# Kernel tuning notes

Measured on AMD Instinct MI355X. Metric: run time of the kernel, lower is better.

## Reference

```python
import jax, jax.numpy as jnp
import numpy as np

B, S, H = 16, 1024, 1024  # S must equal H for the original bmm to type-check


def setup_inputs() -> dict:
    key = jax.random.key(0)
    k1, k2, k3, k4, k5 = jax.random.split(key, 5)
    ht = jax.random.normal(k1, (B, H), dtype=jnp.float32)
    encoder_out = jax.random.normal(k2, (B, S, H), dtype=jnp.float32)
    # nn.Linear(2H, H): weight [H, 2H], bias [H]
    W_attn = jax.random.normal(k3, (H, 2 * H), dtype=jnp.float32) / np.sqrt(2 * H)
    b_attn = jax.random.normal(k4, (H,), dtype=jnp.float32) * 0.01
    # nn.Linear(H, 1, bias=False): weight [1, H]  (computed in forward but its output is discarded)
    W_v = jax.random.normal(k5, (1, H), dtype=jnp.float32) / np.sqrt(H)
    return {"ht": ht, "encoder_out": encoder_out, "W_attn": W_attn, "b_attn": b_attn, "W_v": W_v}


def reference(ht, encoder_out, W_attn, b_attn, W_v):
    b, s, h = encoder_out.shape
    # ht.repeat(S,1,1).transpose(0,1) -> [B,S,H]
    ht_rep = jnp.broadcast_to(ht[:, None, :], (b, s, h))
    energy = jnp.concatenate([ht_rep, encoder_out], axis=2)          # [B,S,2H]
    energy = jnp.tanh(jnp.einsum('bsk,hk->bsh', energy, W_attn) + b_attn)  # [B,S,H]
    # v projection is computed in the original forward but not returned (dead output)
    _attention = jnp.einsum('bsh,oh->bso', energy, W_v)[..., 0]      # [B,S], unused
    # NOTE: softmax over dim=1 (the seq axis) of the full 3D energy, as in the original
    attention_weights = jax.nn.softmax(energy, axis=1)               # [B,S,H]
    # bmm([B,S,H],[B,S,H]) with S==H: contract weights' H axis vs encoder_out's S axis
    context = jnp.einsum('bsk,bkh->bsh', attention_weights, encoder_out)  # [B,S,H]
    return (context, attention_weights)
```

## Files before the change

kernel.cpp:

```cpp
#include <hip/hip_runtime.h>
#include <math.h>

#define Bn 16
#define Sn 1024
#define Hn 1024
static const size_t SH = (size_t)Sn * Hn;
static const size_t BSH = (size_t)Bn * Sn * Hn;

typedef __attribute__((ext_vector_type(8))) short short8;
typedef __attribute__((ext_vector_type(4))) float f32x4;

#define GLD16(gp, lp) __builtin_amdgcn_global_load_lds( \
    (const __attribute__((address_space(1))) void*)(gp), \
    (__attribute__((address_space(3))) void*)(lp), 16, 0, 0)

__device__ __forceinline__ short bfr(float f) {
  union { float f; unsigned u; } v; v.f = f;
  unsigned r = (v.u + 0x7FFFu + ((v.u >> 16) & 1u)) >> 16;
  return (short)r;
}
__device__ __forceinline__ float b2f(unsigned short u) {
  union { unsigned u; float f; } v; v.u = (unsigned)u << 16; return v.f;
}
__device__ __forceinline__ short8 cvt8(float4 x, float4 y) {
  short8 r;
  r[0] = bfr(x.x); r[1] = bfr(x.y); r[2] = bfr(x.z); r[3] = bfr(x.w);
  r[4] = bfr(y.x); r[5] = bfr(y.y); r[6] = bfr(y.z); r[7] = bfr(y.w);
  return r;
}

__device__ __forceinline__ int swz8(int row, int g) {
  return (g & ~7) | ((g & 7) ^ (row & 7));
}

__global__ __launch_bounds__(256) void fused_cvt_kernel(const float* __restrict__ enc,
                                                        short* __restrict__ enc_bf,
                                                        short* __restrict__ encT) {
  __shared__ float tile[64][65];
  const int b = blockIdx.z;
  const int s0 = blockIdx.y * 64, h0 = blockIdx.x * 64;
  const int t = threadIdx.x;
  const int tr = t >> 4, tc = t & 15;
  const float* src = enc + (size_t)b * SH;
#pragma unroll
  for (int i = 0; i < 4; ++i) {
    const int s = i * 16 + tr;
    const float4 v = *(const float4*)(src + (size_t)(s0 + s) * 1024 + h0 + tc * 4);
    tile[s][tc * 4 + 0] = v.x; tile[s][tc * 4 + 1] = v.y;
    tile[s][tc * 4 + 2] = v.z; tile[s][tc * 4 + 3] = v.w;
  }
  __syncthreads();
  {
    const int rloc = t >> 2;
    const int rg = b * 1024 + s0 + rloc;
#pragma unroll
    for (int jj = 0; jj < 2; ++jj) {
      const int jloc = (t & 3) * 2 + jj;
      const int slot = jloc ^ (rg & 7);
      const float4 x = *(const float4*)&tile[rloc][jloc * 8];
      const float4 y = *(const float4*)&tile[rloc][jloc * 8 + 4];
      *(short8*)(enc_bf + (size_t)rg * 1024 + h0 + slot * 8) = cvt8(x, y);
    }
  }
  {
    const int hr = t >> 2, cs = t & 3;
    const int h = h0 + hr;
#pragma unroll
    for (int blk = 0; blk < 2; ++blk) {
      const int sg = blk * 4 + cs;
      const int gl = (s0 >> 3) + sg;
      const int gst = swz8(h, gl);
      short8 pk;
#pragma unroll
      for (int j = 0; j < 8; ++j) pk[j] = bfr(tile[sg * 8 + j][hr]);
      *(short8*)(encT + (size_t)b * SH + (size_t)h * 1024 + gst * 8) = pk;
    }
  }
}

__global__ __launch_bounds__(256) void cvt_enc_kernel(const float* __restrict__ enc,
                                                      short* __restrict__ enc_bf) {
  const int g = blockIdx.x * 256 + threadIdx.x;
  const int row = g >> 7;
  const int cs = g & 127;
  const float4 x = *(const float4*)(enc + (size_t)row * 1024 + cs * 8);
  const float4 y = *(const float4*)(enc + (size_t)row * 1024 + cs * 8 + 4);
  *(short8*)(enc_bf + (size_t)row * 1024 + swz8(row, cs) * 8) = cvt8(x, y);
}

__global__ __launch_bounds__(256) void cvt_w2_kernel(const float* __restrict__ W_attn,
                                                     short* __restrict__ W2_bf) {
  const int g = blockIdx.x * 256 + threadIdx.x;
  const int h = g >> 7;
  const int cs = g & 127;
  const float4 x = *(const float4*)(W_attn + (size_t)h * 2048 + 1024 + cs * 8);
  const float4 y = *(const float4*)(W_attn + (size_t)h * 2048 + 1024 + cs * 8 + 4);
  *(short8*)(W2_bf + (size_t)h * 1024 + swz8(h, cs) * 8) = cvt8(x, y);
}

__global__ __launch_bounds__(256) void c1_kernel(const float* __restrict__ ht,
                                                 const float* __restrict__ W_attn,
                                                 const float* __restrict__ b_attn,
                                                 float* __restrict__ c1) {
  __shared__ float hts[16384];
  const int t = threadIdx.x;
#pragma unroll
  for (int i = 0; i < 16; ++i)
    *(float4*)&hts[i * 1024 + t * 4] = *(const float4*)&ht[i * 1024 + t * 4];
  __syncthreads();
  const int h = blockIdx.x * 4 + (t >> 6);
  const int lane = t & 63;
  const float* w = W_attn + (size_t)h * 2048;
  float s[16];
#pragma unroll
  for (int b = 0; b < 16; ++b) s[b] = 0.f;
  for (int k = lane; k < 1024; k += 64) {
    const float wv = w[k];
#pragma unroll
    for (int b = 0; b < 16; ++b) s[b] = fmaf(wv, hts[b * 1024 + k], s[b]);
  }
#pragma unroll
  for (int b = 0; b < 16; ++b) {
    float v = s[b];
#pragma unroll
    for (int off = 32; off; off >>= 1) v += __shfl_down(v, off, 64);
    if (lane == 0) c1[b * 1024 + h] = v + b_attn[h];
  }
}

#define STAGE_A(kt, mh) do {                                              \
  const int p_ = (kt) & 1;                                                \
  _Pragma("unroll") for (int ld_ = 0; ld_ < 2; ++ld_) {                   \
    const int rl_ = (ld_ * 8 + wid) * 8 + (l >> 3);                       \
    GLD16(Ag + (size_t)((rl_ >> 6) * 128 + (mh) * 64 + (rl_ & 63)) * 1024 \
             + (kt) * 64 + (l & 7) * 8,                                   \
          &lds[p_ * 32768 + (mh) * 8192 + (ld_ * 8 + wid) * 512]);        \
  } } while (0)

#define STAGE_B(kt, nh) do {                                              \
  const int p_ = (kt) & 1;                                                \
  _Pragma("unroll") for (int ld_ = 0; ld_ < 2; ++ld_) {                   \
    const int rl_ = (ld_ * 8 + wid) * 8 + (l >> 3);                       \
    GLD16(Bg + (size_t)((rl_ >> 5) * 64 + (nh) * 32 + (rl_ & 31)) * 1024  \
             + (kt) * 64 + (l & 7) * 8,                                   \
          &lds[16384 + p_ * 32768 + (nh) * 8192 + (ld_ * 8 + wid) * 512]); \
  } } while (0)

#define PHASE(mh, nh, ...) do {                                           \
  if ((nh) == 0) {                                                        \
    _Pragma("unroll") for (int mi = 0; mi < 4; ++mi)                      \
      _Pragma("unroll") for (int ks = 0; ks < 2; ++ks)                    \
        afr[mi][ks] = *(const short8*)&lds[ab + (mh) * 8192               \
            + (wr * 64 + mi * 16 + fr) * 64                               \
            + (((ks * 4 + kg) ^ (fr & 7)) << 3)];                         \
  }                                                                       \
  _Pragma("unroll") for (int ni = 0; ni < 2; ++ni)                        \
    _Pragma("unroll") for (int ks = 0; ks < 2; ++ks)                      \
      bfrg[ni][ks] = *(const short8*)&lds[bb + (nh) * 8192                \
          + (wc * 32 + ni * 16 + fr) * 64                                 \
          + (((ks * 4 + kg) ^ (fr & 7)) << 3)];                           \
  __VA_ARGS__;                                                            \
  __builtin_amdgcn_s_barrier();                                           \
  __builtin_amdgcn_s_setprio(1);                                          \
  _Pragma("unroll") for (int mi = 0; mi < 4; ++mi)                        \
    _Pragma("unroll") for (int ni = 0; ni < 2; ++ni)                      \
      _Pragma("unroll") for (int ks = 0; ks < 2; ++ks)                    \
        acc[(mh) * 4 + mi][(nh) * 2 + ni] =                               \
            __builtin_amdgcn_mfma_f32_16x16x32_bf16(afr[mi][ks],          \
                bfrg[ni][ks], acc[(mh) * 4 + mi][(nh) * 2 + ni], 0, 0, 0); \
  __builtin_amdgcn_s_setprio(0);                                          \
} while (0)

#define KLOOP_8PHASE()                                                    \
  STAGE_A(0, 0); STAGE_B(0, 0); STAGE_B(0, 1); STAGE_A(0, 1);             \
  STAGE_A(1, 0); STAGE_B(1, 0);                                           \
  asm volatile("s_waitcnt vmcnt(4)" ::: "memory");                        \
  __builtin_amdgcn_s_barrier();                                           \
  _Pragma("unroll 2") for (int kt = 0; kt < 16; ++kt) {                   \
    const int ab = (kt & 1) * 32768;                                      \
    const int bb = 16384 + (kt & 1) * 32768;                              \
    PHASE(0, 0, if (kt < 15) STAGE_B(kt + 1, 1));                         \
    __builtin_amdgcn_s_barrier();                                         \
    PHASE(0, 1, if (kt < 15) STAGE_A(kt + 1, 1));                         \
    __builtin_amdgcn_s_barrier();                                         \
    PHASE(1, 0, if (kt < 14) STAGE_A(kt + 2, 0));                         \
    __builtin_amdgcn_s_barrier();                                         \
    PHASE(1, 1, if (kt < 14) STAGE_B(kt + 2, 0));                         \
    if (kt < 14) asm volatile("s_waitcnt vmcnt(4)" ::: "memory");         \
    else         asm volatile("s_waitcnt vmcnt(0)" ::: "memory");         \
    __builtin_amdgcn_s_barrier();                                         \
  }

__global__ __launch_bounds__(512) void energy8(const short* __restrict__ enc_bf,
                                               const short* __restrict__ W2_bf,
                                               const float* __restrict__ c1,
                                               short* __restrict__ Xbf,
                                               float* __restrict__ colsum) {
  __shared__ __align__(16) short lds[65536];
  const int flat = blockIdx.x;
  const int id = (flat & 7) * 32 + (flat >> 3);
  const int b = id >> 4;
  const int row0 = ((id >> 2) & 3) * 256;
  const int col0 = (id & 3) * 256;
  const int t = threadIdx.x;
  const int wid = t >> 6, l = t & 63;
  const int wr = wid >> 2, wc = wid & 3;
  const int fr = l & 15, kg = l >> 4;

  const short* Ag = enc_bf + (size_t)b * SH + (size_t)row0 * 1024;
  const short* Bg = W2_bf + (size_t)col0 * 1024;

  f32x4 acc[8][4] = {};
  short8 afr[4][2], bfrg[2][2];

  KLOOP_8PHASE();
  __syncthreads();

  unsigned short* obuf = (unsigned short*)lds;
#pragma unroll
  for (int n = 0; n < 4; ++n) {
    const int col_loc = wc * 64 + n * 16 + fr;
    const float c1v = c1[b * 1024 + col0 + col_loc];
    float csum = 0.f;
#pragma unroll
    for (int m = 0; m < 8; ++m) {
#pragma unroll
      for (int r = 0; r < 4; ++r) {
        const int row_loc = wr * 128 + m * 16 + kg * 4 + r;
        const float x = acc[m][n][r] + c1v;
        const float e = __expf(2.f * x);
        const float X = __expf((e - 1.f) / (e + 1.f));
        csum += X;
        const int g = col_loc >> 3;
        const int sg = (g & ~7) | ((g & 7) ^ (row_loc & 7));
        obuf[row_loc * 256 + sg * 8 + (col_loc & 7)] = (unsigned short)bfr(X);
      }
    }
    csum += __shfl_xor(csum, 16);
    csum += __shfl_xor(csum, 32);
    if (l < 16) atomicAdd(&colsum[b * 1024 + col0 + col_loc], csum);
  }
  __syncthreads();
  const int orow = t >> 1;
  short* gd = Xbf + (size_t)b * SH + (size_t)(row0 + orow) * 1024 + col0;
#pragma unroll
  for (int j = 0; j < 16; ++j) {
    const int ls = (t & 1) * 16 + j;
    *(short8*)(gd + ls * 8) = *(short8*)&obuf[orow * 256 + ls * 8];
  }
}

__global__ __launch_bounds__(512) void context8(const short* __restrict__ awbf,
                                                const short* __restrict__ encT,
                                                float* __restrict__ ctx) {
  __shared__ __align__(16) short lds[65536];
  const int flat = blockIdx.x;
  const int id = (flat & 7) * 32 + (flat >> 3);
  const int b = id >> 4;
  const int row0 = ((id >> 2) & 3) * 256;
  const int col0 = (id & 3) * 256;
  const int t = threadIdx.x;
  const int wid = t >> 6, l = t & 63;
  const int wr = wid >> 2, wc = wid & 3;
  const int fr = l & 15, kg = l >> 4;

  const short* Ag = awbf + (size_t)b * SH + (size_t)row0 * 1024;
  const short* Bg = encT + (size_t)b * SH + (size_t)col0 * 1024;

  f32x4 acc[8][4] = {};
  short8 afr[4][2], bfrg[2][2];

  KLOOP_8PHASE();

  float* Cb = ctx + (size_t)b * SH;
#pragma unroll
  for (int n = 0; n < 4; ++n) {
    const int col = col0 + wc * 64 + n * 16 + fr;
#pragma unroll
    for (int m = 0; m < 8; ++m) {
#pragma unroll
      for (int r = 0; r < 4; ++r)
        Cb[(size_t)(row0 + wr * 128 + m * 16 + kg * 4 + r) * 1024 + col] = acc[m][n][r];
    }
  }
}

__global__ __launch_bounds__(256) void rcp_kernel(const float* __restrict__ cs,
                                                  float* __restrict__ ci) {
  const int i = blockIdx.x * 256 + threadIdx.x;
  ci[i] = 1.0f / cs[i];
}

__global__ __launch_bounds__(256) void scale_v1(short* __restrict__ Xbf,
                                                const float* __restrict__ colinv,
                                                float* __restrict__ aw) {
  const size_t gid = (size_t)blockIdx.x * 256 + threadIdx.x;
  const int rg = (int)(gid >> 7);
  const int ss = (int)(gid & 127);
  const int b = rg >> 10;
  const int gl = (ss & ~7) | ((ss & 7) ^ (rg & 7));
  const int h0 = gl * 8;
  short* p = Xbf + (size_t)rg * 1024 + ss * 8;
  const short8 v = *(const short8*)p;
  const float4 ci0 = *(const float4*)(colinv + (b << 10) + h0);
  const float4 ci1 = *(const float4*)(colinv + (b << 10) + h0 + 4);
  float f[8];
  f[0] = b2f((unsigned short)v[0]) * ci0.x; f[1] = b2f((unsigned short)v[1]) * ci0.y;
  f[2] = b2f((unsigned short)v[2]) * ci0.z; f[3] = b2f((unsigned short)v[3]) * ci0.w;
  f[4] = b2f((unsigned short)v[4]) * ci1.x; f[5] = b2f((unsigned short)v[5]) * ci1.y;
  f[6] = b2f((unsigned short)v[6]) * ci1.z; f[7] = b2f((unsigned short)v[7]) * ci1.w;
  float4 o0 = {f[0], f[1], f[2], f[3]};
  float4 o1 = {f[4], f[5], f[6], f[7]};
  *(float4*)(aw + (size_t)rg * 1024 + h0) = o0;
  *(float4*)(aw + (size_t)rg * 1024 + h0 + 4) = o1;
  short8 r;
#pragma unroll
  for (int j = 0; j < 8; ++j) r[j] = bfr(f[j]);
  *(short8*)p = r;
}

__global__ __launch_bounds__(256) void energy_mfma4(const short* __restrict__ enc_bf,
                                                    const short* __restrict__ W2_bf,
                                                    const float* __restrict__ c1,
                                                    float* __restrict__ X) {
  __shared__ __align__(16) short Ast[128 * 64];
  __shared__ __align__(16) short Bst[128 * 64];
  const int flat = blockIdx.x + (blockIdx.y << 3) + (blockIdx.z << 6);
  const int swz = (flat & 7) * 128 + (flat >> 3);
  const int b = swz >> 6;
  const int row0 = ((swz >> 3) & 7) * 128;
  const int col0 = (swz & 7) * 128;
  const int t = threadIdx.x;
  const int l = t & 63;
  const int w = t >> 6;
  const int wr = w >> 1, wc = w & 1;
  const int fr = l & 15, kg = l >> 4;

  const short* Abase = enc_bf + (size_t)b * SH + (size_t)(row0 + w * 32 + (l >> 3)) * 1024 + (l & 7) * 8;
  const short* Bbase = W2_bf + (size_t)(col0 + w * 32 + (l >> 3)) * 1024 + (l & 7) * 8;
  short* Alds = Ast + w * 2048;
  short* Blds = Bst + w * 2048;

  f32x4 acc[4][4] = {};

  for (int k0 = 0; k0 < 1024; k0 += 64) {
#pragma unroll
    for (int j = 0; j < 4; ++j) {
      GLD16(Abase + k0 + j * 8 * 1024, Alds + j * 512);
      GLD16(Bbase + k0 + j * 8 * 1024, Blds + j * 512);
    }
    __syncthreads();
#pragma unroll
    for (int kk = 0; kk < 2; ++kk) {
      short8 af[4], bf4[4];
#pragma unroll
      for (int m = 0; m < 4; ++m) {
        const int r = wr * 64 + m * 16 + fr;
        af[m] = *(const short8*)&Ast[r * 64 + (((kk * 4 + kg) ^ (r & 7)) << 3)];
      }
#pragma unroll
      for (int n = 0; n < 4; ++n) {
        const int r = wc * 64 + n * 16 + fr;
        bf4[n] = *(const short8*)&Bst[r * 64 + (((kk * 4 + kg) ^ (r & 7)) << 3)];
      }
#pragma unroll
      for (int m = 0; m < 4; ++m)
#pragma unroll
        for (int n = 0; n < 4; ++n)
          acc[m][n] = __builtin_amdgcn_mfma_f32_16x16x32_bf16(af[m], bf4[n], acc[m][n], 0, 0, 0);
    }
    __syncthreads();
  }

  float* Xb = X + (size_t)b * SH;
#pragma unroll
  for (int n = 0; n < 4; ++n) {
    const int col = col0 + wc * 64 + n * 16 + fr;
    const float c1v = c1[b * 1024 + col];
#pragma unroll
    for (int m = 0; m < 4; ++m) {
      const int r0 = row0 + wr * 64 + m * 16 + kg * 4;
#pragma unroll
      for (int r = 0; r < 4; ++r) {
        const float x = acc[m][n][r] + c1v;
        const float e = __expf(2.f * x);
        Xb[(size_t)(r0 + r) * 1024 + col] = __expf((e - 1.f) / (e + 1.f));
      }
    }
  }
}

__global__ __launch_bounds__(256) void norm_kernel(float* __restrict__ X) {
  const int b = blockIdx.x >> 4;
  const int hg = blockIdx.x & 15;
  const int l = threadIdx.x & 63;
  const int sg = threadIdx.x >> 6;
  float* col = X + (size_t)b * SH + hg * 64 + l;
  const int s0 = sg * 256;
  float sum = 0.f;
#pragma unroll 8
  for (int s = s0; s < s0 + 256; ++s) sum += col[(size_t)s * 1024];
  __shared__ float red[4][64];
  red[sg][l] = sum;
  __syncthreads();
  const float inv = 1.f / (red[0][l] + red[1][l] + red[2][l] + red[3][l]);
#pragma unroll 8
  for (int s = s0; s < s0 + 256; ++s) col[(size_t)s * 1024] *= inv;
}

__global__ __launch_bounds__(256) void context_mfma(const float* __restrict__ aw,
                                                    const float* __restrict__ enc,
                                                    float* __restrict__ ctx) {
  __shared__ __align__(16) short Ast[128 * 32];
  __shared__ __align__(16) short Bst[128 * 32];
  const int b = blockIdx.z;
  const int row0 = blockIdx.y * 128;
  const int col0 = blockIdx.x * 128;
  const int t = threadIdx.x;
  const int l = t & 63;
  const int w = t >> 6;
  const int wr = w >> 1, wc = w & 1;
  const int fr = l & 15, kg = l >> 4;

  const int sr = t >> 1;
  const int sc0 = (t & 1) * 2;
  const float* arow = aw + (size_t)b * SH + (size_t)(row0 + sr) * 1024;
  const int bcol = t & 127;
  const int kb0 = (t >> 7) * 2;
  const float* bcolp = enc + (size_t)b * SH + col0 + bcol;

  f32x4 acc[4][4] = {};

#define LSLOT(r, g) ((r) * 32 + (((g) ^ (((r) >> 1) & 3)) << 3))
  for (int k0 = 0; k0 < 1024; k0 += 32) {
    const float4 a0 = *(const float4*)(arow + k0 + sc0 * 8);
    const float4 a1 = *(const float4*)(arow + k0 + sc0 * 8 + 4);
    const float4 a2 = *(const float4*)(arow + k0 + sc0 * 8 + 8);
    const float4 a3 = *(const float4*)(arow + k0 + sc0 * 8 + 12);
    float bv[2][8];
#pragma unroll
    for (int j = 0; j < 2; ++j)
#pragma unroll
      for (int i = 0; i < 8; ++i)
        bv[j][i] = bcolp[(size_t)(k0 + (kb0 + j) * 8 + i) * 1024];
    __syncthreads();
    *(short8*)&Ast[LSLOT(sr, sc0)]     = cvt8(a0, a1);
    *(short8*)&Ast[LSLOT(sr, sc0 + 1)] = cvt8(a2, a3);
#pragma unroll
    for (int j = 0; j < 2; ++j) {
      short8 pk;
#pragma unroll
      for (int i = 0; i < 8; ++i) pk[i] = bfr(bv[j][i]);
      *(short8*)&Bst[LSLOT(bcol, kb0 + j)] = pk;
    }
    __syncthreads();
    short8 af[4], bf4[4];
#pragma unroll
    for (int m = 0; m < 4; ++m) {
      const int r = wr * 64 + m * 16 + fr;
      af[m] = *(const short8*)&Ast[LSLOT(r, kg)];
    }
#pragma unroll
    for (int n = 0; n < 4; ++n) {
      const int r = wc * 64 + n * 16 + fr;
      bf4[n] = *(const short8*)&Bst[LSLOT(r, kg)];
    }
#pragma unroll
    for (int m = 0; m < 4; ++m)
#pragma unroll
      for (int n = 0; n < 4; ++n)
        acc[m][n] = __builtin_amdgcn_mfma_f32_16x16x32_bf16(af[m], bf4[n], acc[m][n], 0, 0, 0);
  }

  float* Cb = ctx + (size_t)b * SH;
#pragma unroll
  for (int n = 0; n < 4; ++n) {
    const int col = col0 + wc * 64 + n * 16 + fr;
#pragma unroll
    for (int m = 0; m < 4; ++m) {
      const int r0 = row0 + wr * 64 + m * 16 + kg * 4;
#pragma unroll
      for (int r = 0; r < 4; ++r)
        Cb[(size_t)(r0 + r) * 1024 + col] = acc[m][n][r];
    }
  }
}

extern "C" void kernel_launch(void* const* d_in, const int* in_sizes, int n_in,
                              void* d_out, int out_size, void* d_ws, size_t ws_size,
                              hipStream_t stream) {
  (void)in_sizes; (void)n_in; (void)out_size;
  const float* ht     = (const float*)d_in[0];
  const float* enc    = (const float*)d_in[1];
  const float* W_attn = (const float*)d_in[2];
  const float* b_attn = (const float*)d_in[3];

  float* ctx = (float*)d_out;
  float* aw  = ctx + BSH;

  short* enc_bf = (short*)ctx;
  short* W2_bf  = (short*)(ctx + 8388608);
  float* c1f    = ctx + 8912896;
  float* colsum = c1f + 16384;
  float* colinv = c1f + 32768;

  const bool ws2 = ws_size >= ((size_t)64 << 20);
  short* encT = (short*)d_ws;
  short* Xbf  = (short*)((char*)d_ws + ((size_t)32 << 20));

  cvt_w2_kernel<<<512, 256, 0, stream>>>(W_attn, W2_bf);
  c1_kernel<<<Hn / 4, 256, 0, stream>>>(ht, W_attn, b_attn, c1f);

  if (ws2) {
    dim3 gt(16, 16, Bn);
    fused_cvt_kernel<<<gt, 256, 0, stream>>>(enc, enc_bf, encT);
    hipMemsetAsync(colsum, 0, 65536, stream);
    energy8<<<256, 512, 0, stream>>>(enc_bf, W2_bf, c1f, Xbf, colsum);
    rcp_kernel<<<64, 256, 0, stream>>>(colsum, colinv);
    scale_v1<<<8192, 256, 0, stream>>>(Xbf, colinv, aw);
    context8<<<256, 512, 0, stream>>>(Xbf, encT, ctx);
  } else {
    cvt_enc_kernel<<<8192, 256, 0, stream>>>(enc, enc_bf);
    dim3 g(8, 8, Bn);
    energy_mfma4<<<g, 256, 0, stream>>>(enc_bf, W2_bf, c1f, aw);
    norm_kernel<<<Bn * 16, 256, 0, stream>>>(aw);
    context_mfma<<<g, 256, 0, stream>>>(aw, enc, ctx);
  }
}
```

Baseline: 168.7 us.

## Replace 256x256 8-phase energy GEMM with simpler 128x128 tile kernel

Swaps the energy GEMM kernel from 256x256 tiles with 512 threads and an 8-phase double-buffered pipeline for 128x128 tiles with 256 threads and a single-buffered LDS loop. The grid goes from 256 to 1024 blocks, which gives better CU coverage and lets several blocks share a CU with far less LDS each. The cost is less data reuse per tile and no explicit overlap of loads with MFMA inside a block. The tanh, exp, column-sum and bf16 store epilogue is unchanged.

Result: slower. 172.4 us (+2.2%).

```diff
diff --git a/kernel.cpp b/kernel.cpp
--- a/kernel.cpp
+++ b/kernel.cpp
@@ -125,6 +125,94 @@
 #pragma unroll
     for (int off = 32; off; off >>= 1) v += __shfl_down(v, off, 64);
     if (lane == 0) c1[b * 1024 + h] = v + b_attn[h];
+  }
+}
+
+__global__ __launch_bounds__(256) void energy_v3(const short* __restrict__ enc_bf,
+                                                 const short* __restrict__ W2_bf,
+                                                 const float* __restrict__ c1,
+                                                 short* __restrict__ Xbf,
+                                                 float* __restrict__ colsum) {
+  __shared__ __align__(16) short SMEM[2 * 128 * 64];
+  short* Ast = SMEM;
+  short* Bst = SMEM + 128 * 64;
+  const int flat = blockIdx.x + (blockIdx.y << 3) + (blockIdx.z << 6);
+  const int swz = (flat & 7) * 128 + (flat >> 3);
+  const int b = swz >> 6;
+  const int row0 = ((swz >> 3) & 7) * 128;
+  const int col0 = (swz & 7) * 128;
+  const int t = threadIdx.x;
+  const int l = t & 63;
+  const int w = t >> 6;
+  const int wr = w >> 1, wc = w & 1;
+  const int fr = l & 15, kg = l >> 4;
+
+  const short* Abase = enc_bf + (size_t)b * SH + (size_t)(row0 + w * 32 + (l >> 3)) * 1024 + (l & 7) * 8;
+  const short* Bbase = W2_bf + (size_t)(col0 + w * 32 + (l >> 3)) * 1024 + (l & 7) * 8;
+  short* Alds = Ast + w * 2048;
+  short* Blds = Bst + w * 2048;
+
+  f32x4 acc[4][4] = {};
+
+  for (int k0 = 0; k0 < 1024; k0 += 64) {
+#pragma unroll
+    for (int j = 0; j < 4; ++j) {
+      GLD16(Abase + k0 + j * 8 * 1024, Alds + j * 512);
+      GLD16(Bbase + k0 + j * 8 * 1024, Blds + j * 512);
+    }
+    __syncthreads();
+#pragma unroll
+    for (int kk = 0; kk < 2; ++kk) {
+      short8 af[4], bf4[4];
+#pragma unroll
+      for (int m = 0; m < 4; ++m) {
+        const int r = wr * 64 + m * 16 + fr;
+        af[m] = *(const short8*)&Ast[r * 64 + (((kk * 4 + kg) ^ (r & 7)) << 3)];
+      }
+#pragma unroll
+      for (int n = 0; n < 4; ++n) {
+        const int r = wc * 64 + n * 16 + fr;
+        bf4[n] = *(const short8*)&Bst[r * 64 + (((kk * 4 + kg) ^ (r & 7)) << 3)];
+      }
+#pragma unroll
+      for (int m = 0; m < 4; ++m)
+#pragma unroll
+        for (int n = 0; n < 4; ++n)
+          acc[m][n] = __builtin_amdgcn_mfma_f32_16x16x32_bf16(af[m], bf4[n], acc[m][n], 0, 0, 0);
+    }
+    __syncthreads();
+  }
+
+  unsigned short* obuf = (unsigned short*)SMEM;
+#pragma unroll
+  for (int n = 0; n < 4; ++n) {
+    const int col_loc = wc * 64 + n * 16 + fr;
+    const float c1v = c1[b * 1024 + col0 + col_loc];
+    float csum = 0.f;
+#pragma unroll
+    for (int m = 0; m < 4; ++m) {
+      const int rbase = wr * 64 + m * 16 + kg * 4;
+#pragma unroll
+      for (int r = 0; r < 4; ++r) {
+        const float x = acc[m][n][r] + c1v;
+        const float e = __expf(2.f * x);
+        const float X = __expf((e - 1.f) / (e + 1.f));
+        csum += X;
+        const int row = rbase + r;
+        obuf[row * 128 + (col_loc ^ ((row & 7) << 3))] = (unsigned short)bfr(X);
+      }
+    }
+    csum += __shfl_xor(csum, 16);
+    csum += __shfl_xor(csum, 32);
+    if (l < 16) atomicAdd(&colsum[b * 1024 + col0 + col_loc], csum);
+  }
+  __syncthreads();
+  const int orow = t >> 1;
+  short* gdst = Xbf + (size_t)b * SH + (size_t)(row0 + orow) * 1024 + col0;
+#pragma unroll
+  for (int j = 0; j < 8; ++j) {
+    const int slot = (t & 1) * 8 + j;
+    *(short8*)(gdst + slot * 8) = *(short8*)&obuf[orow * 128 + slot * 8];
   }
 }
 
@@ -191,65 +279,6 @@
     __builtin_amdgcn_s_barrier();                                         \
   }
 
-__global__ __launch_bounds__(512) void energy8(const short* __restrict__ enc_bf,
-                                               const short* __restrict__ W2_bf,
-                                               const float* __restrict__ c1,
-                                               short* __restrict__ Xbf,
-                                               float* __restrict__ colsum) {
-  __shared__ __align__(16) short lds[65536];
-  const int flat = blockIdx.x;
-  const int id = (flat & 7) * 32 + (flat >> 3);
-  const int b = id >> 4;
-  const int row0 = ((id >> 2) & 3) * 256;
-  const int col0 = (id & 3) * 256;
-  const int t = threadIdx.x;
-  const int wid = t >> 6, l = t & 63;
-  const int wr = wid >> 2, wc = wid & 3;
-  const int fr = l & 15, kg = l >> 4;
-
-  const short* Ag = enc_bf + (size_t)b * SH + (size_t)row0 * 1024;
-  const short* Bg = W2_bf + (size_t)col0 * 1024;
-
-  f32x4 acc[8][4] = {};
-  short8 afr[4][2], bfrg[2][2];
-
-  KLOOP_8PHASE();
-  __syncthreads();
-
-  unsigned short* obuf = (unsigned short*)lds;
-#pragma unroll
-  for (int n = 0; n < 4; ++n) {
-    const int col_loc = wc * 64 + n * 16 + fr;
-    const float c1v = c1[b * 1024 + col0 + col_loc];
-    float csum = 0.f;
-#pragma unroll
-    for (int m = 0; m < 8; ++m) {
-#pragma unroll
-      for (int r = 0; r < 4; ++r) {
-        const int row_loc = wr * 128 + m * 16 + kg * 4 + r;
-        const float x = acc[m][n][r] + c1v;
-        const float e = __expf(2.f * x);
-        const float X = __expf((e - 1.f) / (e + 1.f));
-        csum += X;
-        const int g = col_loc >> 3;
-        const int sg = (g & ~7) | ((g & 7) ^ (row_loc & 7));
-        obuf[row_loc * 256 + sg * 8 + (col_loc & 7)] = (unsigned short)bfr(X);
-      }
-    }
-    csum += __shfl_xor(csum, 16);
-    csum += __shfl_xor(csum, 32);
-    if (l < 16) atomicAdd(&colsum[b * 1024 + col0 + col_loc], csum);
-  }
-  __syncthreads();
-  const int orow = t >> 1;
-  short* gd = Xbf + (size_t)b * SH + (size_t)(row0 + orow) * 1024 + col0;
-#pragma unroll
-  for (int j = 0; j < 16; ++j) {
-    const int ls = (t & 1) * 16 + j;
-    *(short8*)(gd + ls * 8) = *(short8*)&obuf[orow * 256 + ls * 8];
-  }
-}
-
 __global__ __launch_bounds__(512) void context8(const short* __restrict__ awbf,
                                                 const short* __restrict__ encT,
                                                 float* __restrict__ ctx) {
@@ -515,7 +544,8 @@
     dim3 gt(16, 16, Bn);
     fused_cvt_kernel<<<gt, 256, 0, stream>>>(enc, enc_bf, encT);
     hipMemsetAsync(colsum, 0, 65536, stream);
-    energy8<<<256, 512, 0, stream>>>(enc_bf, W2_bf, c1f, Xbf, colsum);
+    dim3 g(8, 8, Bn);
+    energy_v3<<<g, 256, 0, stream>>>(enc_bf, W2_bf, c1f, Xbf, colsum);
     rcp_kernel<<<64, 256, 0, stream>>>(colsum, colinv);
     scale_v1<<<8192, 256, 0, stream>>>(Xbf, colinv, aw);
     context8<<<256, 512, 0, stream>>>(Xbf, encT, ctx);
```
